# Performance work log

Hardware: AMD Instinct MI355X
Metric: run time of the kernel (lower is better)

Reference implementation:

```python
import jax, jax.numpy as jnp
import numpy as np

D = 256; NH = 8; NL = 4; NP = 4; DFF = 1024
SHAPES = [(100, 100), (50, 50), (25, 25), (13, 13)]
B = 4


def layer_norm(x, g, b, eps=1e-5):
    m = x.mean(-1, keepdims=True)
    v = ((x - m) ** 2).mean(-1, keepdims=True)
    return (x - m) * jax.lax.rsqrt(v + eps) * g + b


def setup_inputs() -> dict:
    key = jax.random.key(0)
    ks = jax.random.split(key, 12)
    Lin = sum(h * w for h, w in SHAPES)  # 13294
    w = lambda k, s: jax.random.normal(k, s, jnp.float32) * 0.02
    return dict(
        src=jax.random.normal(ks[0], (B, Lin, D), jnp.float32),
        pos=0.1 * jax.random.normal(ks[1], (B, Lin, D), jnp.float32),
        reference_points=jax.random.uniform(ks[2], (B, Lin, NL, 2), dtype=jnp.float32),
        spatial_shapes=jnp.array(SHAPES, jnp.int32),
        level_start_index=jnp.array(np.cumsum([0] + [h * w for h, w in SHAPES])[:-1], jnp.int32),
        value_w=w(ks[3], (D, D)), value_b=jnp.zeros((D,), jnp.float32),
        offs_w=w(ks[4], (D, NH * NL * NP * 2)),
        offs_b=0.5 * jax.random.normal(ks[5], (NH * NL * NP * 2,), jnp.float32),
        attn_w=w(ks[6], (D, NH * NL * NP)), attn_b=jnp.zeros((NH * NL * NP,), jnp.float32),
        out_w=w(ks[7], (D, D)), out_b=jnp.zeros((D,), jnp.float32),
        ln1_g=jnp.ones((D,), jnp.float32), ln1_b=jnp.zeros((D,), jnp.float32),
        ff1_w=w(ks[8], (D, DFF)), ff1_b=jnp.zeros((DFF,), jnp.float32),
        ff2_w=w(ks[9], (DFF, D)), ff2_b=jnp.zeros((D,), jnp.float32),
        ln2_g=jnp.ones((D,), jnp.float32), ln2_b=jnp.zeros((D,), jnp.float32),
    )


def msda(query, value_in, ref, shapes, starts, value_w, value_b, offs_w, offs_b,
         attn_w, attn_b, out_w, out_b):
    Bq, Lq, Dm = query.shape
    dh = Dm // NH
    shapes_np = np.asarray(shapes); starts_np = np.asarray(starts)
    value = (value_in @ value_w + value_b).reshape(Bq, -1, NH, dh)
    offs = (query @ offs_w + offs_b).reshape(Bq, Lq, NH, NL, NP, 2)
    aw = jax.nn.softmax((query @ attn_w + attn_b).reshape(Bq, Lq, NH, NL * NP), axis=-1)
    aw = aw.reshape(Bq, Lq, NH, NL, NP)
    # offset normalizer is (W, H) per level
    normalizer = jnp.stack([shapes[:, 1], shapes[:, 0]], -1).astype(jnp.float32)
    loc = ref[:, :, None, :, None, :] + offs / normalizer[None, None, None, :, None, :]
    out = jnp.zeros((Bq, NH, Lq, dh), jnp.float32)
    for l in range(NL):
        Hl, Wl = int(shapes_np[l, 0]), int(shapes_np[l, 1])
        s = int(starts_np[l])
        v = value[:, s:s + Hl * Wl].transpose(0, 2, 1, 3)  # [B,h,HW,dh]
        x = loc[:, :, :, l, :, 0] * Wl - 0.5  # [B,Lq,h,P], align_corners=False
        y = loc[:, :, :, l, :, 1] * Hl - 0.5
        x0 = jnp.floor(x); y0 = jnp.floor(y)
        dx = x - x0; dy = y - y0
        x0i = x0.astype(jnp.int32); y0i = y0.astype(jnp.int32)
        def gather(ix, iy):
            valid = (ix >= 0) & (ix < Wl) & (iy >= 0) & (iy < Hl)  # zero padding
            idx = jnp.clip(iy, 0, Hl - 1) * Wl + jnp.clip(ix, 0, Wl - 1)
            idx = idx.transpose(0, 2, 1, 3).reshape(Bq, NH, Lq * NP)
            g = jnp.take_along_axis(v, idx[..., None], axis=2).reshape(Bq, NH, Lq, NP, dh)
            return g * valid.transpose(0, 2, 1, 3)[..., None]
        dxh = dx.transpose(0, 2, 1, 3)[..., None]
        dyh = dy.transpose(0, 2, 1, 3)[..., None]
        sampled = (gather(x0i, y0i) * (1 - dxh) * (1 - dyh)
                   + gather(x0i + 1, y0i) * dxh * (1 - dyh)
                   + gather(x0i, y0i + 1) * (1 - dxh) * dyh
                   + gather(x0i + 1, y0i + 1) * dxh * dyh)  # [B,h,Lq,P,dh]
        awl = aw[:, :, :, l].transpose(0, 2, 1, 3)[..., None]  # [B,h,Lq,P,1]
        out = out + (sampled * awl).sum(3)
    out = out.transpose(0, 2, 1, 3).reshape(Bq, Lq, Dm)
    return out @ out_w + out_b


def reference(src, pos, reference_points, spatial_shapes, level_start_index,
              value_w, value_b, offs_w, offs_b, attn_w, attn_b, out_w, out_b,
              ln1_g, ln1_b, ff1_w, ff1_b, ff2_w, ff2_b, ln2_g, ln2_b):
    # src = with_pos_embed(src, pos): NOTE this module uses (src + pos) as BOTH query and value
    q = src + pos
    src2 = msda(q, q, reference_points, spatial_shapes, level_start_index,
                value_w, value_b, offs_w, offs_b, attn_w, attn_b, out_w, out_b)
    x = layer_norm(q + src2, ln1_g, ln1_b)  # dropout is identity at eval
    ff = jnp.maximum(x @ ff1_w + ff1_b, 0.0) @ ff2_w + ff2_b
    return layer_norm(x + ff, ln2_g, ln2_b)
```

## Files before the change

kernel.cpp:

```cpp
#include <hip/hip_runtime.h>
#include <hip/hip_bf16.h>

#define B_    4
#define LIN   13294
#define M_    (B_*LIN)
#define D_    256
#define NH_   8
#define NL_   4
#define NP_   4
#define DFF_  1024

typedef __bf16 bf16;
typedef unsigned int uint;
typedef __attribute__((ext_vector_type(8))) __bf16 bfrag8;
typedef __attribute__((ext_vector_type(4))) __bf16 bf16x4;
typedef __attribute__((ext_vector_type(4))) float facc4;
typedef __attribute__((ext_vector_type(2))) float f32x2;

__global__ __launch_bounds__(256) void make_q(const float* __restrict__ src,
                                              const float* __restrict__ pos,
                                              float* __restrict__ q,
                                              bf16* __restrict__ qb, int n4) {
  int i = blockIdx.x * 256 + threadIdx.x;
  if (i >= n4) return;
  float4 s = ((const float4*)src)[i];
  float4 p = ((const float4*)pos)[i];
  float4 v = {s.x + p.x, s.y + p.y, s.z + p.z, s.w + p.w};
  ((float4*)q)[i] = v;
  bf16 t4[4] = {(bf16)v.x, (bf16)v.y, (bf16)v.z, (bf16)v.w};
  ((uint2*)qb)[i] = *(uint2*)t4;
}

__global__ __launch_bounds__(256) void prep_weights(
    const float* __restrict__ vw, const float* __restrict__ ow,
    const float* __restrict__ aw, const float* __restrict__ outw,
    const float* __restrict__ f1w, const float* __restrict__ f2w,
    const float* __restrict__ vb, const float* __restrict__ ob,
    const float* __restrict__ ab,
    bf16* __restrict__ vowt, bf16* __restrict__ outwt,
    bf16* __restrict__ f1wt, bf16* __restrict__ f2wt, float* __restrict__ vobias) {
  int seg = blockIdx.y;
  int idx = blockIdx.x * 256 + threadIdx.x;
  if (seg == 6) {
    if (idx < 256) vobias[idx] = vb[idx];
    else if (idx < 512) vobias[idx] = ob[idx - 256];
    else if (idx < 640) vobias[idx] = ab[idx - 512];
    return;
  }
  const float* W; bf16* Wt; int K, N;
  switch (seg) {
    case 0: W = vw;   Wt = vowt;              K = 256;  N = 256;  break;
    case 1: W = ow;   Wt = vowt + 256 * 256;  K = 256;  N = 256;  break;
    case 2: W = aw;   Wt = vowt + 512 * 256;  K = 256;  N = 128;  break;
    case 3: W = outw; Wt = outwt;             K = 256;  N = 256;  break;
    case 4: W = f1w;  Wt = f1wt;              K = 256;  N = 1024; break;
    default: W = f2w; Wt = f2wt;              K = 1024; N = 256;  break;
  }
  if (idx < K * N) {
    int n = idx / K, k = idx - n * K;
    Wt[idx] = (bf16)W[k * N + n];
  }
}

__device__ __forceinline__ void gload16(const bf16* g, bf16* l) {
  __builtin_amdgcn_global_load_lds(
      (const __attribute__((address_space(1))) uint*)g,
      (__attribute__((address_space(3))) uint*)l, 16, 0, 0);
}

template<int K, bool RELU>
__global__ __launch_bounds__(256) void gemm128(
    const bf16* __restrict__ A, const bf16* __restrict__ Bt,
    const float* __restrict__ bias, bf16* __restrict__ C,
    int Mdim, int N) {
  __shared__ __align__(16) bf16 As[128 * 64];
  __shared__ __align__(16) bf16 Bs[128 * 64];
  const int t = threadIdx.x, wave = t >> 6, lane = t & 63;
  const int m0 = blockIdx.x * 128, n0 = blockIdx.y * 128;
  const int wr = wave >> 1, wc = wave & 1;
  const int ln = lane & 15, quad = lane >> 4;
  const int sr = lane >> 3, cc = lane & 7;
  const int gcol = (cc ^ sr) * 8;

  const bf16* ap[4]; const bf16* bp[4];
  bf16* la[4]; bf16* lb[4];
  #pragma unroll
  for (int ii = 0; ii < 4; ii++) {
    int i = wave * 4 + ii;
    int arow = min(m0 + i * 8 + sr, Mdim - 1);
    ap[ii] = A + (size_t)arow * K + gcol;
    bp[ii] = Bt + (size_t)(n0 + i * 8 + sr) * K + gcol;
    la[ii] = As + i * 512;
    lb[ii] = Bs + i * 512;
  }
  int a_off[4], b_off[4];
  #pragma unroll
  for (int i = 0; i < 4; i++) {
    int ra = wr * 64 + i * 16 + ln;
    int rb = wc * 64 + i * 16 + ln;
    a_off[i] = ra * 128 + ((quad ^ (ra & 7)) * 16);
    b_off[i] = rb * 128 + ((quad ^ (rb & 7)) * 16);
  }

  facc4 acc[4][4];
  #pragma unroll
  for (int mt = 0; mt < 4; mt++)
    #pragma unroll
    for (int nt = 0; nt < 4; nt++) acc[mt][nt] = (facc4){0.f, 0.f, 0.f, 0.f};

  #pragma unroll 1
  for (int k0 = 0; k0 < K; k0 += 64) {
    __syncthreads();
    gload16(ap[0] + k0, la[0]); gload16(ap[1] + k0, la[1]);
    gload16(ap[2] + k0, la[2]); gload16(ap[3] + k0, la[3]);
    gload16(bp[0] + k0, lb[0]); gload16(bp[1] + k0, lb[1]);
    gload16(bp[2] + k0, lb[2]); gload16(bp[3] + k0, lb[3]);
    __syncthreads();
    #pragma unroll
    for (int ks = 0; ks < 2; ks++) {
      bfrag8 wfr[4], xfr[4];
      #pragma unroll
      for (int nt = 0; nt < 4; nt++)
        wfr[nt] = *(const bfrag8*)((const char*)Bs + (b_off[nt] ^ (ks * 64)));
      #pragma unroll
      for (int mt = 0; mt < 4; mt++)
        xfr[mt] = *(const bfrag8*)((const char*)As + (a_off[mt] ^ (ks * 64)));
      #pragma unroll
      for (int mt = 0; mt < 4; mt++)
        #pragma unroll
        for (int nt = 0; nt < 4; nt++)
          acc[mt][nt] = __builtin_amdgcn_mfma_f32_16x16x32_bf16(wfr[nt], xfr[mt], acc[mt][nt], 0, 0, 0);
    }
  }

  #pragma unroll
  for (int nt = 0; nt < 4; nt++) {
    int ncol = n0 + wc * 64 + nt * 16 + quad * 4;
    float4 bv = *(const float4*)&bias[ncol];
    #pragma unroll
    for (int mt = 0; mt < 4; mt++) {
      int row = m0 + wr * 64 + mt * 16 + ln;
      if (row < Mdim) {
        float v0 = acc[mt][nt][0] + bv.x, v1 = acc[mt][nt][1] + bv.y;
        float v2 = acc[mt][nt][2] + bv.z, v3 = acc[mt][nt][3] + bv.w;
        if (RELU) {
          v0 = fmaxf(v0, 0.f); v1 = fmaxf(v1, 0.f);
          v2 = fmaxf(v2, 0.f); v3 = fmaxf(v3, 0.f);
        }
        bf16 o[4] = {(bf16)v0, (bf16)v1, (bf16)v2, (bf16)v3};
        *(uint2*)&C[(size_t)row * N + ncol] = *(uint2*)o;
      }
    }
  }
}

__device__ __forceinline__ void corner_acc(const bf16* p, float cw, f32x2 acc2[4]) {
  const uint4 vv = *(const uint4*)p;
  f32x2 cw2 = {cw, cw};
  f32x2 v0 = {__uint_as_float(vv.x << 16), __uint_as_float(vv.x & 0xffff0000u)};
  f32x2 v1 = {__uint_as_float(vv.y << 16), __uint_as_float(vv.y & 0xffff0000u)};
  f32x2 v2 = {__uint_as_float(vv.z << 16), __uint_as_float(vv.z & 0xffff0000u)};
  f32x2 v3 = {__uint_as_float(vv.w << 16), __uint_as_float(vv.w & 0xffff0000u)};
  acc2[0] = cw2 * v0 + acc2[0];
  acc2[1] = cw2 * v1 + acc2[1];
  acc2[2] = cw2 * v2 + acc2[2];
  acc2[3] = cw2 * v3 + acc2[3];
}

__global__ __launch_bounds__(256) void msda_sample(
    const bf16* __restrict__ VOA,
    const float* __restrict__ ref,
    bf16* __restrict__ sampled) {
  int gw = (blockIdx.x * 256 + threadIdx.x) >> 6;
  int lane = threadIdx.x & 63;
  int m = gw >> 3, h = gw & 7;
  if (m >= M_) return;
  int b = m / LIN;
  int p = lane >> 2, cg = lane & 3;
  int l = p >> 2, pt = p & 3;
  int Wl = (l == 0) ? 100 : (l == 1) ? 50 : (l == 2) ? 25 : 13;
  int Hl = Wl;
  int st = (l == 0) ? 0 : (l == 1) ? 10000 : (l == 2) ? 12500 : 13125;

  const bf16* row = VOA + (size_t)m * 640;
  float e = __expf((float)row[512 + h * 16 + p]);
  float se = e;
  #pragma unroll
  for (int msk = 4; msk < 64; msk <<= 1) se += __shfl_xor(se, msk);
  float w = e / se;

  float rx = ref[((size_t)m * 4 + l) * 2 + 0];
  float ry = ref[((size_t)m * 4 + l) * 2 + 1];
  uint oxy = *(const uint*)&row[256 + ((h * 4 + l) * 4 + pt) * 2];
  float ox = __uint_as_float(oxy << 16);
  float oy = __uint_as_float(oxy & 0xffff0000u);
  float x = rx * (float)Wl + ox - 0.5f;
  float y = ry * (float)Hl + oy - 0.5f;
  float x0f = floorf(x), y0f = floorf(y);
  float dx = x - x0f, dy = y - y0f;
  int x0 = (int)x0f, y0 = (int)y0f;

  int xc0 = min(max(x0, 0), Wl - 1), xc1 = min(max(x0 + 1, 0), Wl - 1);
  int yc0 = min(max(y0, 0), Hl - 1), yc1 = min(max(y0 + 1, 0), Hl - 1);
  bool vx0 = (x0 >= 0) & (x0 < Wl);
  bool vx1 = (x0 + 1 >= 0) & (x0 + 1 < Wl);
  bool vy0 = (y0 >= 0) & (y0 < Hl);
  bool vy1 = (y0 + 1 >= 0) & (y0 + 1 < Hl);
  float wxa = vx0 ? (1.f - dx) : 0.f;
  float wxb = vx1 ? dx : 0.f;
  float wya = (vy0 ? (1.f - dy) : 0.f) * w;
  float wyb = (vy1 ? dy : 0.f) * w;
  uint ys = (uint)(Wl * 640);
  uint xoa = (uint)xc0 * 640u, xob = (uint)xc1 * 640u;
  uint yoa = (uint)yc0 * ys,   yob = (uint)yc1 * ys;

  const bf16* vb0 = VOA + ((size_t)(b * LIN + st)) * 640 + h * 32 + cg * 8;

  f32x2 acc2[4];
  #pragma unroll
  for (int i = 0; i < 4; i++) acc2[i] = (f32x2){0.f, 0.f};

  corner_acc(vb0 + yoa + xoa, wxa * wya, acc2);
  corner_acc(vb0 + yoa + xob, wxb * wya, acc2);
  corner_acc(vb0 + yob + xoa, wxa * wyb, acc2);
  corner_acc(vb0 + yob + xob, wxb * wyb, acc2);

  int sel = (lane >> 2) & 1;
  f32x2 sA0 = sel ? acc2[0] : acc2[2];
  f32x2 sA1 = sel ? acc2[1] : acc2[3];
  f32x2 kA0 = sel ? acc2[2] : acc2[0];
  f32x2 kA1 = sel ? acc2[3] : acc2[1];
  f32x2 rA0, rA1;
  rA0.x = __shfl_xor(sA0.x, 4); rA0.y = __shfl_xor(sA0.y, 4);
  rA1.x = __shfl_xor(sA1.x, 4); rA1.y = __shfl_xor(sA1.y, 4);
  kA0 += rA0; kA1 += rA1;

  int sel2 = (lane >> 3) & 1;
  f32x2 sB = sel2 ? kA0 : kA1;
  f32x2 kB = sel2 ? kA1 : kA0;
  f32x2 rB;
  rB.x = __shfl_xor(sB.x, 8); rB.y = __shfl_xor(sB.y, 8);
  kB += rB;

  int sel3 = (lane >> 4) & 1;
  float sC = sel3 ? kB.x : kB.y;
  float kC = sel3 ? kB.y : kB.x;
  kC += __shfl_xor(sC, 16);

  float v = kC + __shfl_xor(kC, 32);

  if (lane < 32) {
    int c = cg * 8 + ((lane >> 2) & 1) * 4 + ((lane >> 3) & 1) * 2 + ((lane >> 4) & 1);
    sampled[(size_t)m * 256 + h * 32 + c] = (bf16)v;
  }
}

__device__ inline float4 load4f(const float* p) { return *(const float4*)p; }
__device__ inline float4 load4f(const bf16* p) {
  bf16x4 v = *(const bf16x4*)p;
  float4 r = {(float)v[0], (float)v[1], (float)v[2], (float)v[3]};
  return r;
}
template<typename RT>
__global__ __launch_bounds__(256) void ln_kernel(
    const bf16* __restrict__ a, const RT* __restrict__ res,
    const float* __restrict__ g, const float* __restrict__ beta,
    float* __restrict__ out_f, bf16* __restrict__ out_b, int Mdim) {
  int wave = threadIdx.x >> 6, lane = threadIdx.x & 63;
  int row = blockIdx.x * 4 + wave;
  if (row >= Mdim) return;
  size_t base = (size_t)row * 256 + lane * 4;
  float4 av = load4f(a + base);
  float4 rv = load4f(res + base);
  float4 v = {av.x + rv.x, av.y + rv.y, av.z + rv.z, av.w + rv.w};
  float s = v.x + v.y + v.z + v.w;
  #pragma unroll
  for (int msk = 1; msk < 64; msk <<= 1) s += __shfl_xor(s, msk);
  float mean = s * (1.f / 256.f);
  float4 d = {v.x - mean, v.y - mean, v.z - mean, v.w - mean};
  float sq = d.x * d.x + d.y * d.y + d.z * d.z + d.w * d.w;
  #pragma unroll
  for (int msk = 1; msk < 64; msk <<= 1) sq += __shfl_xor(sq, msk);
  float inv = rsqrtf(sq * (1.f / 256.f) + 1e-5f);
  float4 gv = *(const float4*)(g + lane * 4);
  float4 bv = *(const float4*)(beta + lane * 4);
  float4 y = {d.x * inv * gv.x + bv.x, d.y * inv * gv.y + bv.y,
              d.z * inv * gv.z + bv.z, d.w * inv * gv.w + bv.w};
  if (out_f) *(float4*)(out_f + base) = y;
  if (out_b) {
    bf16 t4[4] = {(bf16)y.x, (bf16)y.y, (bf16)y.z, (bf16)y.w};
    *(uint2*)(out_b + base) = *(uint2*)t4;
  }
}

extern "C" void kernel_launch(void* const* d_in, const int* in_sizes, int n_in,
                              void* d_out, int out_size, void* d_ws, size_t ws_size,
                              hipStream_t stream) {
  const float* src     = (const float*)d_in[0];
  const float* pos     = (const float*)d_in[1];
  const float* refpts  = (const float*)d_in[2];
  const float* value_w = (const float*)d_in[5];
  const float* value_b = (const float*)d_in[6];
  const float* offs_w  = (const float*)d_in[7];
  const float* offs_b  = (const float*)d_in[8];
  const float* attn_w  = (const float*)d_in[9];
  const float* attn_b  = (const float*)d_in[10];
  const float* out_w   = (const float*)d_in[11];
  const float* out_b   = (const float*)d_in[12];
  const float* ln1_g   = (const float*)d_in[13];
  const float* ln1_b   = (const float*)d_in[14];
  const float* ff1_w   = (const float*)d_in[15];
  const float* ff1_b   = (const float*)d_in[16];
  const float* ff2_w   = (const float*)d_in[17];
  const float* ff2_b   = (const float*)d_in[18];
  const float* ln2_g   = (const float*)d_in[19];
  const float* ln2_b   = (const float*)d_in[20];

  char* ws = (char*)d_ws;
  size_t off = 0;
  auto take = [&](size_t bytes) -> char* {
    char* pp = ws + off;
    off += (bytes + 255) & ~(size_t)255;
    return pp;
  };
  float* q      = (float*)take((size_t)M_ * 256 * 4);
  size_t szQB   = (size_t)M_ * 256 * 2;
  size_t szVOA  = (size_t)M_ * 640 * 2;
  char* R       = take(szQB + szVOA + szQB);
  bf16* qb      = (bf16*)R;
  bf16* VOA     = (bf16*)(R + szQB);
  bf16* sampled = (bf16*)(R + szQB + szVOA);
  bf16* hb      = (bf16*)R;
  bf16* tmp     = (bf16*)take(szQB);
  bf16* x       = (bf16*)take(szQB);
  bf16* vowt    = (bf16*)take(640 * 256 * 2);
  bf16* outwt   = (bf16*)take(65536 * 2);
  bf16* f1wt    = (bf16*)take(262144 * 2);
  bf16* f2wt    = (bf16*)take(262144 * 2);
  float* vobias = (float*)take(640 * 4);
  (void)ws_size; (void)in_sizes; (void)n_in; (void)out_size;

  int n4 = M_ * 256 / 4;
  make_q<<<dim3((n4 + 255) / 256), dim3(256), 0, stream>>>(src, pos, q, qb, n4);
  prep_weights<<<dim3(1024, 7), dim3(256), 0, stream>>>(
      value_w, offs_w, attn_w, out_w, ff1_w, ff2_w, value_b, offs_b, attn_b,
      vowt, outwt, f1wt, f2wt, vobias);

  dim3 blk(256);
  int mt = (M_ + 127) / 128;
  gemm128<256, false><<<dim3(mt, 5), blk, 0, stream>>>(qb, vowt, vobias, VOA, M_, 640);
  msda_sample<<<dim3(M_ * 2), blk, 0, stream>>>(VOA, refpts, sampled);
  gemm128<256, false><<<dim3(mt, 2), blk, 0, stream>>>(sampled, outwt, out_b, tmp, M_, 256);
  ln_kernel<float><<<dim3((M_ + 3) / 4), blk, 0, stream>>>(tmp, q, ln1_g, ln1_b, nullptr, x, M_);
  gemm128<256, true><<<dim3(mt, 8), blk, 0, stream>>>(x, f1wt, ff1_b, hb, M_, 1024);
  gemm128<1024, false><<<dim3(mt, 2), blk, 0, stream>>>(hb, f2wt, ff2_b, tmp, M_, 256);
  ln_kernel<bf16><<<dim3((M_ + 3) / 4), blk, 0, stream>>>(tmp, x, ln2_g, ln2_b, (float*)d_out, nullptr, M_);
}
```

Measured before the change: 583.8 us.

## Process one query per block with half-wave per head in MSDA sampling

Restructures the deformable-attention sampling kernel so each 32-lane half-wave handles one head, with each lane loading 16 channels (two 16-byte loads) per bilinear corner instead of 8. One block now covers all 8 heads of a query, so the grid is halved and the softmax and reduction shuffles span 32 lanes rather than 64. This is meant to cut per-point index, weight and softmax arithmetic and shuffle work, and to let every lane write an output. In exchange each thread holds more accumulator registers and issues more loads.

```diff
diff --git a/kernel.cpp b/kernel.cpp
--- a/kernel.cpp
+++ b/kernel.cpp
@@ -154,39 +154,44 @@
   }
 }
 
-__device__ __forceinline__ void corner_acc(const bf16* p, float cw, f32x2 acc2[4]) {
-  const uint4 vv = *(const uint4*)p;
+#define UNPK(u) (f32x2){__uint_as_float((u) << 16), __uint_as_float((u) & 0xffff0000u)}
+
+__device__ __forceinline__ void corner_acc2(const bf16* pA, float cw, f32x2* acc2) {
+  const uint4 A = *(const uint4*)pA;
+  const uint4 B = *(const uint4*)(pA + 8);
   f32x2 cw2 = {cw, cw};
-  f32x2 v0 = {__uint_as_float(vv.x << 16), __uint_as_float(vv.x & 0xffff0000u)};
-  f32x2 v1 = {__uint_as_float(vv.y << 16), __uint_as_float(vv.y & 0xffff0000u)};
-  f32x2 v2 = {__uint_as_float(vv.z << 16), __uint_as_float(vv.z & 0xffff0000u)};
-  f32x2 v3 = {__uint_as_float(vv.w << 16), __uint_as_float(vv.w & 0xffff0000u)};
-  acc2[0] = cw2 * v0 + acc2[0];
-  acc2[1] = cw2 * v1 + acc2[1];
-  acc2[2] = cw2 * v2 + acc2[2];
-  acc2[3] = cw2 * v3 + acc2[3];
+  acc2[0] = cw2 * UNPK(A.x) + acc2[0];
+  acc2[1] = cw2 * UNPK(A.y) + acc2[1];
+  acc2[2] = cw2 * UNPK(A.z) + acc2[2];
+  acc2[3] = cw2 * UNPK(A.w) + acc2[3];
+  acc2[4] = cw2 * UNPK(B.x) + acc2[4];
+  acc2[5] = cw2 * UNPK(B.y) + acc2[5];
+  acc2[6] = cw2 * UNPK(B.z) + acc2[6];
+  acc2[7] = cw2 * UNPK(B.w) + acc2[7];
 }
 
 __global__ __launch_bounds__(256) void msda_sample(
     const bf16* __restrict__ VOA,
     const float* __restrict__ ref,
     bf16* __restrict__ sampled) {
-  int gw = (blockIdx.x * 256 + threadIdx.x) >> 6;
-  int lane = threadIdx.x & 63;
-  int m = gw >> 3, h = gw & 7;
-  if (m >= M_) return;
-  int b = m / LIN;
-  int p = lane >> 2, cg = lane & 3;
+  int m = blockIdx.x;
+  int wave = threadIdx.x >> 6, lane = threadIdx.x & 63;
+  int h = wave * 2 + (lane >> 5);
+  int lane5 = lane & 31;
+  int p = lane5 >> 1, cg = lane5 & 1;
   int l = p >> 2, pt = p & 3;
   int Wl = (l == 0) ? 100 : (l == 1) ? 50 : (l == 2) ? 25 : 13;
   int Hl = Wl;
   int st = (l == 0) ? 0 : (l == 1) ? 10000 : (l == 2) ? 12500 : 13125;
+  int b = m / LIN;
 
   const bf16* row = VOA + (size_t)m * 640;
   float e = __expf((float)row[512 + h * 16 + p]);
   float se = e;
-  #pragma unroll
-  for (int msk = 4; msk < 64; msk <<= 1) se += __shfl_xor(se, msk);
+  se += __shfl_xor(se, 2);
+  se += __shfl_xor(se, 4);
+  se += __shfl_xor(se, 8);
+  se += __shfl_xor(se, 16);
   float w = e / se;
 
   float rx = ref[((size_t)m * 4 + l) * 2 + 0];
@@ -214,45 +219,51 @@
   uint xoa = (uint)xc0 * 640u, xob = (uint)xc1 * 640u;
   uint yoa = (uint)yc0 * ys,   yob = (uint)yc1 * ys;
 
-  const bf16* vb0 = VOA + ((size_t)(b * LIN + st)) * 640 + h * 32 + cg * 8;
-
-  f32x2 acc2[4];
-  #pragma unroll
-  for (int i = 0; i < 4; i++) acc2[i] = (f32x2){0.f, 0.f};
-
-  corner_acc(vb0 + yoa + xoa, wxa * wya, acc2);
-  corner_acc(vb0 + yoa + xob, wxb * wya, acc2);
-  corner_acc(vb0 + yob + xoa, wxa * wyb, acc2);
-  corner_acc(vb0 + yob + xob, wxb * wyb, acc2);
-
-  int sel = (lane >> 2) & 1;
-  f32x2 sA0 = sel ? acc2[0] : acc2[2];
-  f32x2 sA1 = sel ? acc2[1] : acc2[3];
-  f32x2 kA0 = sel ? acc2[2] : acc2[0];
-  f32x2 kA1 = sel ? acc2[3] : acc2[1];
-  f32x2 rA0, rA1;
-  rA0.x = __shfl_xor(sA0.x, 4); rA0.y = __shfl_xor(sA0.y, 4);
-  rA1.x = __shfl_xor(sA1.x, 4); rA1.y = __shfl_xor(sA1.y, 4);
-  kA0 += rA0; kA1 += rA1;
-
-  int sel2 = (lane >> 3) & 1;
-  f32x2 sB = sel2 ? kA0 : kA1;
-  f32x2 kB = sel2 ? kA1 : kA0;
-  f32x2 rB;
-  rB.x = __shfl_xor(sB.x, 8); rB.y = __shfl_xor(sB.y, 8);
-  kB += rB;
-
-  int sel3 = (lane >> 4) & 1;
-  float sC = sel3 ? kB.x : kB.y;
-  float kC = sel3 ? kB.y : kB.x;
-  kC += __shfl_xor(sC, 16);
-
-  float v = kC + __shfl_xor(kC, 32);
-
-  if (lane < 32) {
-    int c = cg * 8 + ((lane >> 2) & 1) * 4 + ((lane >> 3) & 1) * 2 + ((lane >> 4) & 1);
-    sampled[(size_t)m * 256 + h * 32 + c] = (bf16)v;
-  }
+  const bf16* vb0 = VOA + ((size_t)(b * LIN + st)) * 640 + h * 32 + cg * 16;
+
+  f32x2 acc2[8];
+  #pragma unroll
+  for (int i = 0; i < 8; i++) acc2[i] = (f32x2){0.f, 0.f};
+
+  corner_acc2(vb0 + yoa + xoa, wxa * wya, acc2);
+  corner_acc2(vb0 + yoa + xob, wxb * wya, acc2);
+  corner_acc2(vb0 + yob + xoa, wxa * wyb, acc2);
+  corner_acc2(vb0 + yob + xob, wxb * wyb, acc2);
+
+  int s1 = (lane >> 1) & 1;
+  f32x2 sa0 = s1 ? acc2[0] : acc2[4];
+  f32x2 sa1 = s1 ? acc2[1] : acc2[5];
+  f32x2 sa2 = s1 ? acc2[2] : acc2[6];
+  f32x2 sa3 = s1 ? acc2[3] : acc2[7];
+  f32x2 ka0 = s1 ? acc2[4] : acc2[0];
+  f32x2 ka1 = s1 ? acc2[5] : acc2[1];
+  f32x2 ka2 = s1 ? acc2[6] : acc2[2];
+  f32x2 ka3 = s1 ? acc2[7] : acc2[3];
+  ka0.x += __shfl_xor(sa0.x, 2); ka0.y += __shfl_xor(sa0.y, 2);
+  ka1.x += __shfl_xor(sa1.x, 2); ka1.y += __shfl_xor(sa1.y, 2);
+  ka2.x += __shfl_xor(sa2.x, 2); ka2.y += __shfl_xor(sa2.y, 2);
+  ka3.x += __shfl_xor(sa3.x, 2); ka3.y += __shfl_xor(sa3.y, 2);
+
+  int s2 = (lane >> 2) & 1;
+  f32x2 tb0 = s2 ? ka0 : ka2;
+  f32x2 tb1 = s2 ? ka1 : ka3;
+  f32x2 kb0 = s2 ? ka2 : ka0;
+  f32x2 kb1 = s2 ? ka3 : ka1;
+  kb0.x += __shfl_xor(tb0.x, 4); kb0.y += __shfl_xor(tb0.y, 4);
+  kb1.x += __shfl_xor(tb1.x, 4); kb1.y += __shfl_xor(tb1.y, 4);
+
+  int s3 = (lane >> 3) & 1;
+  f32x2 tc = s3 ? kb0 : kb1;
+  f32x2 kc = s3 ? kb1 : kb0;
+  kc.x += __shfl_xor(tc.x, 8); kc.y += __shfl_xor(tc.y, 8);
+
+  int s4 = (lane >> 4) & 1;
+  float td = s4 ? kc.x : kc.y;
+  float kd = s4 ? kc.y : kc.x;
+  kd += __shfl_xor(td, 16);
+
+  int col = cg * 16 + s1 * 8 + s2 * 4 + s3 * 2 + s4;
+  sampled[(size_t)m * 256 + h * 32 + col] = (bf16)kd;
 }
 
 __device__ inline float4 load4f(const float* p) { return *(const float4*)p; }
@@ -349,7 +360,7 @@
   dim3 blk(256);
   int mt = (M_ + 127) / 128;
   gemm128<256, false><<<dim3(mt, 5), blk, 0, stream>>>(qb, vowt, vobias, VOA, M_, 640);
-  msda_sample<<<dim3(M_ * 2), blk, 0, stream>>>(VOA, refpts, sampled);
+  msda_sample<<<dim3(M_), blk, 0, stream>>>(VOA, refpts, sampled);
   gemm128<256, false><<<dim3(mt, 2), blk, 0, stream>>>(sampled, outwt, out_b, tmp, M_, 256);
   ln_kernel<float><<<dim3((M_ + 3) / 4), blk, 0, stream>>>(tmp, q, ln1_g, ln1_b, nullptr, x, M_);
   gemm128<256, true><<<dim3(mt, 8), blk, 0, stream>>>(x, f1wt, ff1_b, hb, M_, 1024);
```

Measured after the change: 543.4 us. 1.07x faster.
